# Performance work log

Hardware: AMD Instinct MI355X
Metric: run time of the kernel (lower is better)

The kernel has to match this reference:

```python
import jax, jax.numpy as jnp
import numpy as np

N_QUBITS = 6
N_LAYERS = 3
DIM = 2 ** N_QUBITS  # 64

# PauliZ sign table: signs[s, q] = +1 if bit q of basis state s is 0 else -1
# (wire 0 is the most-significant bit, matching pennylane default.qubit)
_IDX = np.arange(DIM)
SIGNS = np.stack([1.0 - 2.0 * ((_IDX >> (N_QUBITS - 1 - q)) & 1) for q in range(N_QUBITS)], axis=1).astype(np.float32)  # (64, 6)


def _rx_mat(theta):  # theta: (B,) -> (B,2,2) complex64
    c = jnp.cos(theta / 2).astype(jnp.complex64)
    s = (-1j * jnp.sin(theta / 2)).astype(jnp.complex64)
    return jnp.stack([jnp.stack([c, s], -1), jnp.stack([s, c], -1)], -2)


def _ry_mat(theta):  # theta: (B,) -> (B,2,2) complex64
    c = jnp.cos(theta / 2).astype(jnp.complex64)
    s = jnp.sin(theta / 2).astype(jnp.complex64)
    return jnp.stack([jnp.stack([c, -s], -1), jnp.stack([s, c], -1)], -2)


def _rz_mat(theta):  # theta: (B,) -> (B,2,2) complex64 (diagonal)
    z = jnp.zeros_like(theta).astype(jnp.complex64)
    e0 = jnp.exp(-1j * theta.astype(jnp.complex64) / 2)
    e1 = jnp.exp(1j * theta.astype(jnp.complex64) / 2)
    return jnp.stack([jnp.stack([e0, z], -1), jnp.stack([z, e1], -1)], -2)


def _apply_1q(state, U, w):
    # state: (B, 64); U: (B,2,2) batched or (2,2) shared; gate on wire w
    B = state.shape[0]
    st = state.reshape(B, 2 ** w, 2, 2 ** (N_QUBITS - 1 - w))
    if U.ndim == 3:
        st = jnp.einsum('bij,bajc->baic', U, st)
    else:
        st = jnp.einsum('ij,bajc->baic', U, st)
    return st.reshape(B, DIM)


def _cnot(state, c, t):
    # CNOT with control wire c, target wire t (fixed structure, batched over B)
    B = state.shape[0]
    s = state.reshape((B,) + (2,) * N_QUBITS)
    ac, at = c + 1, t + 1
    s0 = jnp.take(s, 0, axis=ac)
    s1 = jnp.take(s, 1, axis=ac)
    at2 = at - 1 if at > ac else at  # axis shift after removing control axis
    s1 = jnp.flip(s1, axis=at2)      # X on target when control == 1
    s = jnp.stack([s0, s1], axis=ac)
    return s.reshape(B, DIM)


def simulate(x6, q_weights):
    # x6: (B, 6) angles; q_weights: (3, 6). Returns PauliZ expvals (B, 6).
    B = x6.shape[0]
    state = jnp.zeros((B, DIM), dtype=jnp.complex64).at[:, 0].set(1.0)
    # input encoding: RX, RY, RZ on each wire with rolled input angles
    for i in range(N_QUBITS):
        state = _apply_1q(state, _rx_mat(x6[:, i % N_QUBITS]), i)
        state = _apply_1q(state, _ry_mat(x6[:, (i + 1) % N_QUBITS]), i)
        state = _apply_1q(state, _rz_mat(x6[:, (i + 2) % N_QUBITS]), i)
    # variational layers: RY(weights) then ring of CNOTs
    for l in range(N_LAYERS):
        for q in range(N_QUBITS):
            th = q_weights[l, q]
            c = jnp.cos(th / 2).astype(jnp.complex64)
            s = jnp.sin(th / 2).astype(jnp.complex64)
            U = jnp.stack([jnp.stack([c, -s]), jnp.stack([s, c])])  # (2,2)
            state = _apply_1q(state, U, q)
        for q in range(N_QUBITS):
            state = _cnot(state, q, (q + 1) % N_QUBITS)
    probs = (state.real ** 2 + state.imag ** 2)  # (B, 64) float32
    return probs @ jnp.asarray(SIGNS)            # (B, 6)


def setup_inputs() -> dict:
    key = jax.random.key(0)
    k1, k2, k3, k4 = jax.random.split(key, 4)
    B, H = 32768, 1024
    x = jax.random.normal(k1, (B, N_QUBITS), dtype=jnp.float32)
    hx = jax.random.normal(k2, (B, H), dtype=jnp.float32)
    q_weights = jax.random.uniform(k3, (N_LAYERS, N_QUBITS), dtype=jnp.float32, minval=0.0, maxval=2.0 * np.pi)
    bound = 1.0 / np.sqrt(N_QUBITS)
    fc_w = jax.random.uniform(k4, (H, N_QUBITS), dtype=jnp.float32, minval=-bound, maxval=bound)
    fc_b = jax.random.uniform(jax.random.fold_in(k4, 1), (H,), dtype=jnp.float32, minval=-bound, maxval=bound)
    return {"x": x, "hx": hx, "q_weights": q_weights, "fc_w": fc_w, "fc_b": fc_b}


def reference(x, hx, q_weights, fc_w, fc_b):
    q = simulate(x[:, :N_QUBITS], q_weights)      # (B, 6) PauliZ expvals
    return hx + q @ fc_w.T + fc_b                 # residual + linear
```

## Files before the change

### kernel.cpp

```cpp
#include <hip/hip_runtime.h>


#define NQ 6

typedef float floatx4 __attribute__((ext_vector_type(4)));

__device__ __forceinline__ float rl(float v, int lane) {
    return __int_as_float(__builtin_amdgcn_readlane(__float_as_int(v), lane));
}

__global__ __launch_bounds__(256, 4) void qrnn_fused_kernel(
    const float* __restrict__ x,
    const float* __restrict__ hx,
    const float* __restrict__ qw,
    const float* __restrict__ fc_w,
    const float* __restrict__ fc_b,
    float* __restrict__ out)
{
    const int tid = threadIdx.x;
    const int l   = tid & 63;
    const int wv  = tid >> 6;
    const int bid = blockIdx.x;

    __shared__ float q6s[2][4][6];

    const float4* w4 = (const float4*)fc_w;
    const int h4 = wv * 64 + l;
    const int wb = h4 * 6;
    const float4 a0 = w4[wb + 0], a1 = w4[wb + 1], a2 = w4[wb + 2];
    const float4 a3 = w4[wb + 3], a4 = w4[wb + 4], a5 = w4[wb + 5];
    const float4 bv = ((const float4*)fc_b)[h4];

    float angq = (l >= 6 && l < 24) ? qw[l - 6] : 0.f;
    float saq, caq;
    __sincosf(angq * 0.5f, &saq, &caq);
    float cQ[3][6], sQ[3][6];
    #pragma unroll
    for (int lay = 0; lay < 3; ++lay)
        #pragma unroll
        for (int q = 0; q < 6; ++q) {
            cQ[lay][q] = rl(caq, 6 + lay * 6 + q);
            sQ[lay][q] = rl(saq, 6 + lay * 6 + q);
        }

    int src = l;
    #pragma unroll
    for (int q = 5; q >= 0; --q) {
        const int cb = 5 - q, tb = 5 - ((q + 1) % 6);
        src ^= ((src >> cb) & 1) << tb;
    }
    const int srcl = (l < 6) ? (32 >> l) : 0;

    const float4* hx4 = (const float4*)hx;
    floatx4* out4 = (floatx4*)out;

    #pragma unroll 1
    for (int it = 0; it < 4; ++it) {
        const int r0 = bid * 16 + it * 4;
        const int b  = r0 + wv;

        const float angx = (l < 6) ? x[(size_t)b * NQ + l] : 0.f;

        float4 hv0 = hx4[(size_t)(r0 + 0) * 256 + h4];
        float4 hv1 = hx4[(size_t)(r0 + 1) * 256 + h4];
        float4 hv2 = hx4[(size_t)(r0 + 2) * 256 + h4];
        float4 hv3 = hx4[(size_t)(r0 + 3) * 256 + h4];

        float sax, cax;
        __sincosf(angx * 0.5f, &sax, &cax);
        float cx[6], sx[6];
        #pragma unroll
        for (int i = 0; i < 6; ++i) { cx[i] = rl(cax, i); sx[i] = rl(sax, i); }

        float re = (l == 0) ? 1.f : 0.f;
        float im = 0.f;

        #pragma unroll
        for (int w = 0; w < 6; ++w) {
            const int m = 1 << (5 - w);
            const float sgn = (l & m) ? 1.f : -1.f;
            float pr = __shfl_xor(re, m), pi = __shfl_xor(im, m);
            float c = cx[w], s = sx[w];
            float nr = c * re + s * pi;
            float ni = c * im - s * pr;
            re = nr; im = ni;
            pr = __shfl_xor(re, m); pi = __shfl_xor(im, m);
            c = cx[(w + 1) % 6]; s = sx[(w + 1) % 6] * sgn;
            nr = c * re + s * pr;
            ni = c * im + s * pi;
            re = nr; im = ni;
            c = cx[(w + 2) % 6];
            const float sg = (l & m) ? -sx[(w + 2) % 6] : sx[(w + 2) % 6];
            nr = c * re + sg * im;
            ni = c * im - sg * re;
            re = nr; im = ni;
        }

        #pragma unroll
        for (int lay = 0; lay < 3; ++lay) {
            #pragma unroll
            for (int q = 0; q < 6; ++q) {
                const int m = 1 << (5 - q);
                const float c = cQ[lay][q];
                const float s = sQ[lay][q];
                const float sg = (l & m) ? s : -s;
                const float pr = __shfl_xor(re, m), pi = __shfl_xor(im, m);
                const float nr = c * re + sg * pr;
                const float ni = c * im + sg * pi;
                re = nr; im = ni;
            }
            re = __shfl(re, src);
            im = __shfl(im, src);
        }

        float p = re * re + im * im;
        #pragma unroll
        for (int k = 0; k < 6; ++k) {
            const int m = 1 << k;
            const float t = __shfl_xor(p, m);
            p = (l & m) ? (t - p) : (t + p);
        }
        const float v = __shfl(p, srcl);
        if (l < 6) q6s[it & 1][wv][l] = v;
        __syncthreads();

        #pragma unroll
        for (int r = 0; r < 4; ++r) {
            const float* qb = q6s[it & 1][r];
            const float q0 = qb[0], q1 = qb[1], q2 = qb[2];
            const float q3 = qb[3], q4 = qb[4], q5 = qb[5];
            const float4 hvk = (r == 0) ? hv0 : (r == 1) ? hv1 : (r == 2) ? hv2 : hv3;
            floatx4 res;
            res.x = hvk.x + bv.x + q0*a0.x + q1*a0.y + q2*a0.z + q3*a0.w + q4*a1.x + q5*a1.y;
            res.y = hvk.y + bv.y + q0*a1.z + q1*a1.w + q2*a2.x + q3*a2.y + q4*a2.z + q5*a2.w;
            res.z = hvk.z + bv.z + q0*a3.x + q1*a3.y + q2*a3.z + q3*a3.w + q4*a4.x + q5*a4.y;
            res.w = hvk.w + bv.w + q0*a4.z + q1*a4.w + q2*a5.x + q3*a5.y + q4*a5.z + q5*a5.w;
            __builtin_nontemporal_store(res, &out4[(size_t)(r0 + r) * 256 + h4]);
        }
    }
}

extern "C" void kernel_launch(void* const* d_in, const int* in_sizes, int n_in,
                              void* d_out, int out_size, void* d_ws, size_t ws_size,
                              hipStream_t stream) {
    const float* x    = (const float*)d_in[0];
    const float* hx   = (const float*)d_in[1];
    const float* qw   = (const float*)d_in[2];
    const float* fc_w = (const float*)d_in[3];
    const float* fc_b = (const float*)d_in[4];
    float* out = (float*)d_out;

    const int B = in_sizes[0] / NQ;

    qrnn_fused_kernel<<<B / 16, 256, 0, stream>>>(x, hx, qw, fc_w, fc_b, out);
}
```

Measured before the change: 248.6 us.

## Make each wave own eight rows and drop shared memory and block barrier

Each wavefront now simulates eight batch rows (strided by 4096) on its own and keeps the expectation values in registers, read back with readlane. This removes the shared-memory exchange and the __syncthreads per iteration. The output pass loops over four column chunks per row and software-pipelines hx loads two rows ahead, while the next row's x angles are prefetched during simulation. The grid is fixed at 1024 blocks, which hardcodes B=32768, and fc_w/fc_b are reloaded per chunk instead of being held in registers.

```diff
diff --git a/kernel.cpp b/kernel.cpp
--- a/kernel.cpp
+++ b/kernel.cpp
@@ -20,18 +20,21 @@
     const int tid = threadIdx.x;
     const int l   = tid & 63;
     const int wv  = tid >> 6;
-    const int bid = blockIdx.x;
+    const int w   = blockIdx.x * 4 + wv;
 
-    __shared__ float q6s[2][4][6];
+    const float4* hx4 = (const float4*)hx;
+    const float4* w4  = (const float4*)fc_w;
+    const float4* b4  = (const float4*)fc_b;
+    floatx4* out4 = (floatx4*)out;
 
-    const float4* w4 = (const float4*)fc_w;
-    const int h4 = wv * 64 + l;
-    const int wb = h4 * 6;
-    const float4 a0 = w4[wb + 0], a1 = w4[wb + 1], a2 = w4[wb + 2];
-    const float4 a3 = w4[wb + 3], a4 = w4[wb + 4], a5 = w4[wb + 5];
-    const float4 bv = ((const float4*)fc_b)[h4];
+    const int c0 = l;
+    const float4 pa0 = w4[c0 * 6 + 0], pa1 = w4[c0 * 6 + 1], pa2 = w4[c0 * 6 + 2];
+    const float4 pa3 = w4[c0 * 6 + 3], pa4 = w4[c0 * 6 + 4], pa5 = w4[c0 * 6 + 5];
+    const float4 pbv = b4[c0];
+    const float4 ph0 = hx4[(size_t)(w + 0 * 4096) * 256 + c0];
+    const float4 ph1 = hx4[(size_t)(w + 1 * 4096) * 256 + c0];
 
-    float angq = (l >= 6 && l < 24) ? qw[l - 6] : 0.f;
+    const float angq = (l >= 6 && l < 24) ? qw[l - 6] : 0.f;
     float saq, caq;
     __sincosf(angq * 0.5f, &saq, &caq);
     float cQ[3][6], sQ[3][6];
@@ -51,23 +54,15 @@
     }
     const int srcl = (l < 6) ? (32 >> l) : 0;
 
-    const float4* hx4 = (const float4*)hx;
-    floatx4* out4 = (floatx4*)out;
-
-    #pragma unroll 1
-    for (int it = 0; it < 4; ++it) {
-        const int r0 = bid * 16 + it * 4;
-        const int b  = r0 + wv;
-
-        const float angx = (l < 6) ? x[(size_t)b * NQ + l] : 0.f;
-
-        float4 hv0 = hx4[(size_t)(r0 + 0) * 256 + h4];
-        float4 hv1 = hx4[(size_t)(r0 + 1) * 256 + h4];
-        float4 hv2 = hx4[(size_t)(r0 + 2) * 256 + h4];
-        float4 hv3 = hx4[(size_t)(r0 + 3) * 256 + h4];
+    float qv[8];
+    float curang = (l < 6) ? x[(size_t)w * NQ + l] : 0.f;
+    #pragma unroll
+    for (int k = 0; k < 8; ++k) {
+        const float nextang = (k < 7 && l < 6)
+            ? x[(size_t)(w + (k + 1) * 4096) * NQ + l] : 0.f;
 
         float sax, cax;
-        __sincosf(angx * 0.5f, &sax, &cax);
+        __sincosf(curang * 0.5f, &sax, &cax);
         float cx[6], sx[6];
         #pragma unroll
         for (int i = 0; i < 6; ++i) { cx[i] = rl(cax, i); sx[i] = rl(sax, i); }
@@ -76,21 +71,21 @@
         float im = 0.f;
 
         #pragma unroll
-        for (int w = 0; w < 6; ++w) {
-            const int m = 1 << (5 - w);
+        for (int ww = 0; ww < 6; ++ww) {
+            const int m = 1 << (5 - ww);
             const float sgn = (l & m) ? 1.f : -1.f;
             float pr = __shfl_xor(re, m), pi = __shfl_xor(im, m);
-            float c = cx[w], s = sx[w];
+            float c = cx[ww], s = sx[ww];
             float nr = c * re + s * pi;
             float ni = c * im - s * pr;
             re = nr; im = ni;
             pr = __shfl_xor(re, m); pi = __shfl_xor(im, m);
-            c = cx[(w + 1) % 6]; s = sx[(w + 1) % 6] * sgn;
+            c = cx[(ww + 1) % 6]; s = sx[(ww + 1) % 6] * sgn;
             nr = c * re + s * pr;
             ni = c * im + s * pi;
             re = nr; im = ni;
-            c = cx[(w + 2) % 6];
-            const float sg = (l & m) ? -sx[(w + 2) % 6] : sx[(w + 2) % 6];
+            c = cx[(ww + 2) % 6];
+            const float sg = (l & m) ? -sx[(ww + 2) % 6] : sx[(ww + 2) % 6];
             nr = c * re + sg * im;
             ni = c * im - sg * re;
             re = nr; im = ni;
@@ -115,27 +110,43 @@
 
         float p = re * re + im * im;
         #pragma unroll
-        for (int k = 0; k < 6; ++k) {
-            const int m = 1 << k;
+        for (int kk = 0; kk < 6; ++kk) {
+            const int m = 1 << kk;
             const float t = __shfl_xor(p, m);
             p = (l & m) ? (t - p) : (t + p);
         }
-        const float v = __shfl(p, srcl);
-        if (l < 6) q6s[it & 1][wv][l] = v;
-        __syncthreads();
+        qv[k] = __shfl(p, srcl);
+        curang = nextang;
+    }
 
+    #pragma unroll
+    for (int c = 0; c < 4; ++c) {
+        const int cb = c * 64 + l;
+        float4 a0, a1, a2, a3, a4, a5, bv, h0, h1;
+        if (c == 0) {
+            a0 = pa0; a1 = pa1; a2 = pa2; a3 = pa3; a4 = pa4; a5 = pa5;
+            bv = pbv; h0 = ph0; h1 = ph1;
+        } else {
+            a0 = w4[cb * 6 + 0]; a1 = w4[cb * 6 + 1]; a2 = w4[cb * 6 + 2];
+            a3 = w4[cb * 6 + 3]; a4 = w4[cb * 6 + 4]; a5 = w4[cb * 6 + 5];
+            bv = b4[cb];
+            h0 = hx4[(size_t)(w + 0 * 4096) * 256 + cb];
+            h1 = hx4[(size_t)(w + 1 * 4096) * 256 + cb];
+        }
         #pragma unroll
-        for (int r = 0; r < 4; ++r) {
-            const float* qb = q6s[it & 1][r];
-            const float q0 = qb[0], q1 = qb[1], q2 = qb[2];
-            const float q3 = qb[3], q4 = qb[4], q5 = qb[5];
-            const float4 hvk = (r == 0) ? hv0 : (r == 1) ? hv1 : (r == 2) ? hv2 : hv3;
+        for (int k = 0; k < 8; ++k) {
+            float4 hn = {0.f, 0.f, 0.f, 0.f};
+            if (k < 6) hn = hx4[(size_t)(w + (k + 2) * 4096) * 256 + cb];
+
+            const float q0 = rl(qv[k], 0), q1 = rl(qv[k], 1), q2 = rl(qv[k], 2);
+            const float q3 = rl(qv[k], 3), q4 = rl(qv[k], 4), q5 = rl(qv[k], 5);
             floatx4 res;
-            res.x = hvk.x + bv.x + q0*a0.x + q1*a0.y + q2*a0.z + q3*a0.w + q4*a1.x + q5*a1.y;
-            res.y = hvk.y + bv.y + q0*a1.z + q1*a1.w + q2*a2.x + q3*a2.y + q4*a2.z + q5*a2.w;
-            res.z = hvk.z + bv.z + q0*a3.x + q1*a3.y + q2*a3.z + q3*a3.w + q4*a4.x + q5*a4.y;
-            res.w = hvk.w + bv.w + q0*a4.z + q1*a4.w + q2*a5.x + q3*a5.y + q4*a5.z + q5*a5.w;
-            __builtin_nontemporal_store(res, &out4[(size_t)(r0 + r) * 256 + h4]);
+            res.x = h0.x + bv.x + q0*a0.x + q1*a0.y + q2*a0.z + q3*a0.w + q4*a1.x + q5*a1.y;
+            res.y = h0.y + bv.y + q0*a1.z + q1*a1.w + q2*a2.x + q3*a2.y + q4*a2.z + q5*a2.w;
+            res.z = h0.z + bv.z + q0*a3.x + q1*a3.y + q2*a3.z + q3*a3.w + q4*a4.x + q5*a4.y;
+            res.w = h0.w + bv.w + q0*a4.z + q1*a4.w + q2*a5.x + q3*a5.y + q4*a5.z + q5*a5.w;
+            __builtin_nontemporal_store(res, &out4[(size_t)(w + k * 4096) * 256 + cb]);
+            h0 = h1; h1 = hn;
         }
     }
 }
@@ -150,7 +161,7 @@
     const float* fc_b = (const float*)d_in[4];
     float* out = (float*)d_out;
 
-    const int B = in_sizes[0] / NQ;
+    (void)in_sizes; (void)d_ws; (void)ws_size;
 
-    qrnn_fused_kernel<<<B / 16, 256, 0, stream>>>(x, hx, qw, fc_w, fc_b, out);
+    qrnn_fused_kernel<<<1024, 256, 0, stream>>>(x, hx, qw, fc_w, fc_b, out);
 }
```

After: 276.1 us. 1.11x slower.

## Assign one batch row per wavefront and drop shared-memory exchange

Applied to the files above, without the earlier changes.

Each wavefront now simulates its own row and writes that row's full 1024-wide output in four chunks, reading the six expectation values straight from lanes instead of going through shared memory and __syncthreads. The grid grows from B/16 to B/4 blocks, and each wave software-pipelines the fc_w, fc_b and hx loads one chunk ahead. This removes the block barrier and the per-iteration serial loop. In exchange every wave reloads all of fc_w (a cached 24KB), and there are more blocks with less work per block.

```diff
diff --git a/kernel.cpp b/kernel.cpp
--- a/kernel.cpp
+++ b/kernel.cpp
@@ -20,122 +20,109 @@
     const int tid = threadIdx.x;
     const int l   = tid & 63;
     const int wv  = tid >> 6;
-    const int bid = blockIdx.x;
+    const int r   = blockIdx.x * 4 + wv;
 
-    __shared__ float q6s[2][4][6];
+    const float4* hx4 = (const float4*)hx;
+    const float4* w4  = (const float4*)fc_w;
+    const float4* b4  = (const float4*)fc_b;
+    floatx4* out4 = (floatx4*)out;
 
-    const float4* w4 = (const float4*)fc_w;
-    const int h4 = wv * 64 + l;
-    const int wb = h4 * 6;
-    const float4 a0 = w4[wb + 0], a1 = w4[wb + 1], a2 = w4[wb + 2];
-    const float4 a3 = w4[wb + 3], a4 = w4[wb + 4], a5 = w4[wb + 5];
-    const float4 bv = ((const float4*)fc_b)[h4];
+    const float angx = (l < 6) ? x[(size_t)r * NQ + l] : 0.f;
+    int cb = l;
+    float4 a0 = w4[cb * 6 + 0], a1 = w4[cb * 6 + 1], a2 = w4[cb * 6 + 2];
+    float4 a3 = w4[cb * 6 + 3], a4 = w4[cb * 6 + 4], a5 = w4[cb * 6 + 5];
+    float4 bv = b4[cb];
+    float4 h  = hx4[(size_t)r * 256 + cb];
 
-    float angq = (l >= 6 && l < 24) ? qw[l - 6] : 0.f;
+    const float angq = (l >= 6 && l < 24) ? qw[l - 6] : 0.f;
     float saq, caq;
     __sincosf(angq * 0.5f, &saq, &caq);
-    float cQ[3][6], sQ[3][6];
+
+    float sax, cax;
+    __sincosf(angx * 0.5f, &sax, &cax);
+    float cx[6], sx[6];
     #pragma unroll
-    for (int lay = 0; lay < 3; ++lay)
-        #pragma unroll
-        for (int q = 0; q < 6; ++q) {
-            cQ[lay][q] = rl(caq, 6 + lay * 6 + q);
-            sQ[lay][q] = rl(saq, 6 + lay * 6 + q);
-        }
+    for (int i = 0; i < 6; ++i) { cx[i] = rl(cax, i); sx[i] = rl(sax, i); }
+
+    float re = (l == 0) ? 1.f : 0.f;
+    float im = 0.f;
+
+    #pragma unroll
+    for (int w = 0; w < 6; ++w) {
+        const int m = 1 << (5 - w);
+        const float sgn = (l & m) ? 1.f : -1.f;
+        float pr = __shfl_xor(re, m), pi = __shfl_xor(im, m);
+        float c = cx[w], s = sx[w];
+        float nr = c * re + s * pi;
+        float ni = c * im - s * pr;
+        re = nr; im = ni;
+        pr = __shfl_xor(re, m); pi = __shfl_xor(im, m);
+        c = cx[(w + 1) % 6]; s = sx[(w + 1) % 6] * sgn;
+        nr = c * re + s * pr;
+        ni = c * im + s * pi;
+        re = nr; im = ni;
+        c = cx[(w + 2) % 6];
+        const float sg = (l & m) ? -sx[(w + 2) % 6] : sx[(w + 2) % 6];
+        nr = c * re + sg * im;
+        ni = c * im - sg * re;
+        re = nr; im = ni;
+    }
 
     int src = l;
     #pragma unroll
     for (int q = 5; q >= 0; --q) {
-        const int cb = 5 - q, tb = 5 - ((q + 1) % 6);
-        src ^= ((src >> cb) & 1) << tb;
+        const int cbit = 5 - q, tbit = 5 - ((q + 1) % 6);
+        src ^= ((src >> cbit) & 1) << tbit;
+    }
+
+    #pragma unroll
+    for (int lay = 0; lay < 3; ++lay) {
+        #pragma unroll
+        for (int q = 0; q < 6; ++q) {
+            const int m = 1 << (5 - q);
+            const float c = rl(caq, 6 + lay * 6 + q);
+            const float s = rl(saq, 6 + lay * 6 + q);
+            const float sg = (l & m) ? s : -s;
+            const float pr = __shfl_xor(re, m), pi = __shfl_xor(im, m);
+            const float nr = c * re + sg * pr;
+            const float ni = c * im + sg * pi;
+            re = nr; im = ni;
+        }
+        re = __shfl(re, src);
+        im = __shfl(im, src);
+    }
+
+    float p = re * re + im * im;
+    #pragma unroll
+    for (int k = 0; k < 6; ++k) {
+        const int m = 1 << k;
+        const float t = __shfl_xor(p, m);
+        p = (l & m) ? (t - p) : (t + p);
     }
     const int srcl = (l < 6) ? (32 >> l) : 0;
+    const float qv = __shfl(p, srcl);
+    const float q0 = rl(qv, 0), q1 = rl(qv, 1), q2 = rl(qv, 2);
+    const float q3 = rl(qv, 3), q4 = rl(qv, 4), q5 = rl(qv, 5);
 
-    const float4* hx4 = (const float4*)hx;
-    floatx4* out4 = (floatx4*)out;
-
-    #pragma unroll 1
-    for (int it = 0; it < 4; ++it) {
-        const int r0 = bid * 16 + it * 4;
-        const int b  = r0 + wv;
-
-        const float angx = (l < 6) ? x[(size_t)b * NQ + l] : 0.f;
-
-        float4 hv0 = hx4[(size_t)(r0 + 0) * 256 + h4];
-        float4 hv1 = hx4[(size_t)(r0 + 1) * 256 + h4];
-        float4 hv2 = hx4[(size_t)(r0 + 2) * 256 + h4];
-        float4 hv3 = hx4[(size_t)(r0 + 3) * 256 + h4];
-
-        float sax, cax;
-        __sincosf(angx * 0.5f, &sax, &cax);
-        float cx[6], sx[6];
-        #pragma unroll
-        for (int i = 0; i < 6; ++i) { cx[i] = rl(cax, i); sx[i] = rl(sax, i); }
-
-        float re = (l == 0) ? 1.f : 0.f;
-        float im = 0.f;
-
-        #pragma unroll
-        for (int w = 0; w < 6; ++w) {
-            const int m = 1 << (5 - w);
-            const float sgn = (l & m) ? 1.f : -1.f;
-            float pr = __shfl_xor(re, m), pi = __shfl_xor(im, m);
-            float c = cx[w], s = sx[w];
-            float nr = c * re + s * pi;
-            float ni = c * im - s * pr;
-            re = nr; im = ni;
-            pr = __shfl_xor(re, m); pi = __shfl_xor(im, m);
-            c = cx[(w + 1) % 6]; s = sx[(w + 1) % 6] * sgn;
-            nr = c * re + s * pr;
-            ni = c * im + s * pi;
-            re = nr; im = ni;
-            c = cx[(w + 2) % 6];
-            const float sg = (l & m) ? -sx[(w + 2) % 6] : sx[(w + 2) % 6];
-            nr = c * re + sg * im;
-            ni = c * im - sg * re;
-            re = nr; im = ni;
+    #pragma unroll
+    for (int c = 0; c < 4; ++c) {
+        float4 na0, na1, na2, na3, na4, na5, nbv, nh;
+        if (c < 3) {
+            const int nc = (c + 1) * 64 + l;
+            na0 = w4[nc * 6 + 0]; na1 = w4[nc * 6 + 1]; na2 = w4[nc * 6 + 2];
+            na3 = w4[nc * 6 + 3]; na4 = w4[nc * 6 + 4]; na5 = w4[nc * 6 + 5];
+            nbv = b4[nc];
+            nh  = hx4[(size_t)r * 256 + nc];
         }
-
-        #pragma unroll
-        for (int lay = 0; lay < 3; ++lay) {
-            #pragma unroll
-            for (int q = 0; q < 6; ++q) {
-                const int m = 1 << (5 - q);
-                const float c = cQ[lay][q];
-                const float s = sQ[lay][q];
-                const float sg = (l & m) ? s : -s;
-                const float pr = __shfl_xor(re, m), pi = __shfl_xor(im, m);
-                const float nr = c * re + sg * pr;
-                const float ni = c * im + sg * pi;
-                re = nr; im = ni;
-            }
-            re = __shfl(re, src);
-            im = __shfl(im, src);
-        }
-
-        float p = re * re + im * im;
-        #pragma unroll
-        for (int k = 0; k < 6; ++k) {
-            const int m = 1 << k;
-            const float t = __shfl_xor(p, m);
-            p = (l & m) ? (t - p) : (t + p);
-        }
-        const float v = __shfl(p, srcl);
-        if (l < 6) q6s[it & 1][wv][l] = v;
-        __syncthreads();
-
-        #pragma unroll
-        for (int r = 0; r < 4; ++r) {
-            const float* qb = q6s[it & 1][r];
-            const float q0 = qb[0], q1 = qb[1], q2 = qb[2];
-            const float q3 = qb[3], q4 = qb[4], q5 = qb[5];
-            const float4 hvk = (r == 0) ? hv0 : (r == 1) ? hv1 : (r == 2) ? hv2 : hv3;
-            floatx4 res;
-            res.x = hvk.x + bv.x + q0*a0.x + q1*a0.y + q2*a0.z + q3*a0.w + q4*a1.x + q5*a1.y;
-            res.y = hvk.y + bv.y + q0*a1.z + q1*a1.w + q2*a2.x + q3*a2.y + q4*a2.z + q5*a2.w;
-            res.z = hvk.z + bv.z + q0*a3.x + q1*a3.y + q2*a3.z + q3*a3.w + q4*a4.x + q5*a4.y;
-            res.w = hvk.w + bv.w + q0*a4.z + q1*a4.w + q2*a5.x + q3*a5.y + q4*a5.z + q5*a5.w;
-            __builtin_nontemporal_store(res, &out4[(size_t)(r0 + r) * 256 + h4]);
+        floatx4 res;
+        res.x = h.x + bv.x + q0*a0.x + q1*a0.y + q2*a0.z + q3*a0.w + q4*a1.x + q5*a1.y;
+        res.y = h.y + bv.y + q0*a1.z + q1*a1.w + q2*a2.x + q3*a2.y + q4*a2.z + q5*a2.w;
+        res.z = h.z + bv.z + q0*a3.x + q1*a3.y + q2*a3.z + q3*a3.w + q4*a4.x + q5*a4.y;
+        res.w = h.w + bv.w + q0*a4.z + q1*a4.w + q2*a5.x + q3*a5.y + q4*a5.z + q5*a5.w;
+        __builtin_nontemporal_store(res, &out4[(size_t)r * 256 + c * 64 + l]);
+        if (c < 3) {
+            a0 = na0; a1 = na1; a2 = na2; a3 = na3; a4 = na4; a5 = na5;
+            bv = nbv; h = nh;
         }
     }
 }
@@ -151,6 +138,7 @@
     float* out = (float*)d_out;
 
     const int B = in_sizes[0] / NQ;
+    (void)d_ws; (void)ws_size;
 
-    qrnn_fused_kernel<<<B / 16, 256, 0, stream>>>(x, hx, qw, fc_w, fc_b, out);
+    qrnn_fused_kernel<<<B / 4, 256, 0, stream>>>(x, hx, qw, fc_w, fc_b, out);
 }
```

After: 284.1 us. 14.3% more time.
